# Kernel tuning notes

Measured on AMD Instinct MI355X. Metric: run time of the kernel, lower is better.

The kernel has to match this reference:

```python
import jax, jax.numpy as jnp
import numpy as np

DIM = 1024
NUM_HEADS = 16
NUM_KV_HEADS = 2
HEAD_DIM = DIM // NUM_HEADS          # 64
REPEATS = NUM_HEADS // NUM_KV_HEADS  # 8
WINDOW = 256
HALF = WINDOW // 2                   # 128
BATCH, SEQ = 2, 2048


def setup_inputs() -> dict:
    key = jax.random.key(0)
    ks = jax.random.split(key, 9)
    sc = 1.0 / np.sqrt(DIM)
    return {
        "x":  jax.random.normal(ks[0], (BATCH, SEQ, DIM), jnp.float32),
        "Wq": jax.random.normal(ks[1], (DIM, NUM_HEADS * HEAD_DIM), jnp.float32) * sc,
        "bq": jax.random.normal(ks[2], (NUM_HEADS * HEAD_DIM,), jnp.float32) * 0.01,
        "Wk": jax.random.normal(ks[3], (DIM, NUM_KV_HEADS * HEAD_DIM), jnp.float32) * sc,
        "bk": jax.random.normal(ks[4], (NUM_KV_HEADS * HEAD_DIM,), jnp.float32) * 0.01,
        "Wv": jax.random.normal(ks[5], (DIM, NUM_KV_HEADS * HEAD_DIM), jnp.float32) * sc,
        "bv": jax.random.normal(ks[6], (NUM_KV_HEADS * HEAD_DIM,), jnp.float32) * 0.01,
        "Wo": jax.random.normal(ks[7], (DIM, DIM), jnp.float32) * sc,
        "bo": jax.random.normal(ks[8], (DIM,), jnp.float32) * 0.01,
    }


def reference(x, Wq, bq, Wk, bk, Wv, bv, Wo, bo):
    # Training-path GQA sliding-window attention (faithful to the torch module):
    #  - K/V zero-padded by HALF on each side of the sequence; window of size
    #    WINDOW centered on each query position (unfold with step 1).
    #  - NOTE (faithful): the original code builds mask = tril(ones)[-1], which is
    #    an all-ones row, so masked_fill is a no-op -> NO causal mask inside the
    #    window; padded positions contribute score 0 (not -inf) to the softmax.
    #  - NOTE (faithful): the training path does NOT scale scores by 1/sqrt(d).
    b, s, _ = x.shape
    q = (x @ Wq + bq).reshape(b, s, NUM_HEADS, HEAD_DIM).transpose(0, 2, 1, 3)      # [b,H,s,d]
    k = (x @ Wk + bk).reshape(b, s, NUM_KV_HEADS, HEAD_DIM).transpose(0, 2, 1, 3)   # [b,G,s,d]
    v = (x @ Wv + bv).reshape(b, s, NUM_KV_HEADS, HEAD_DIM).transpose(0, 2, 1, 3)

    kp = jnp.pad(k, ((0, 0), (0, 0), (HALF, HALF), (0, 0)))  # [b,G,s+W,d]
    vp = jnp.pad(v, ((0, 0), (0, 0), (HALF, HALF), (0, 0)))

    # window gather indices: window i covers padded positions [i, i+W)
    idx = jnp.arange(s)[:, None] + jnp.arange(WINDOW)[None, :]  # [s,W]
    k_win = kp[:, :, idx]  # [b,G,s,W,d]  (gather at kv-head granularity, not H)
    v_win = vp[:, :, idx]

    # group query heads by kv head: head h -> kv group h // REPEATS
    qg = q.reshape(b, NUM_KV_HEADS, REPEATS, s, HEAD_DIM)        # [b,G,r,s,d]
    scores = jnp.einsum('bgrsd,bgswd->bgrsw', qg, k_win)         # no scaling (faithful)
    probs = jax.nn.softmax(scores, axis=-1)
    out = jnp.einsum('bgrsw,bgswd->bgrsd', probs, v_win)         # [b,G,r,s,d]

    out = out.reshape(b, NUM_HEADS, s, HEAD_DIM).transpose(0, 2, 1, 3).reshape(b, s, DIM)
    return out @ Wo + bo
```

## Files before the change

kernel.cpp:

```cpp
#include <hip/hip_runtime.h>
#include <hip/hip_fp16.h>

typedef _Float16 h16;
typedef __attribute__((ext_vector_type(4))) _Float16 h16x4;
typedef __attribute__((ext_vector_type(8))) _Float16 h16x8;
typedef __attribute__((ext_vector_type(4))) float f32x4;

#define DIM   1024
#define SEQ   2048
#define NKV   2
#define HD    64
#define HALFW 128
#define NQKV  1280
#define SPAD  2304
#define KPS   (SPAD*HD)
#define KSTG  288
#define VSTR  312
#define PSTR  296
#define LOG2E 1.4426950408889634f

__global__ void preprocess_kernel(const float* __restrict__ x,
                                  const float* __restrict__ bq,
                                  const float* __restrict__ bk,
                                  const float* __restrict__ bv,
                                  const float* __restrict__ Wq,
                                  const float* __restrict__ Wk,
                                  const float* __restrict__ Wv,
                                  const float* __restrict__ Wo,
                                  h16* __restrict__ xh, float* __restrict__ bqkv,
                                  h16* __restrict__ wqkvt, h16* __restrict__ wot,
                                  h16* __restrict__ kpad, h16* __restrict__ vtpad)
{
    __shared__ float tile[32][33];
    const int tid = threadIdx.x;
    const int blk = blockIdx.x;
    if (blk < 2048) {
        int i = blk * 256 + tid;
        size_t base = (size_t)i * 8;
        float4 a = *(const float4*)(x + base);
        float4 b = *(const float4*)(x + base + 4);
        h16x8 o = { (h16)a.x,(h16)a.y,(h16)a.z,(h16)a.w,
                    (h16)b.x,(h16)b.y,(h16)b.z,(h16)b.w };
        *(h16x8*)(xh + base) = o;
        if (i < NQKV) {
            float v = (i < DIM) ? bq[i] * LOG2E
                                : (i < DIM+128 ? bk[i-DIM] : bv[i-DIM-128]);
            bqkv[i] = v;
        }
        return;
    }
    if (blk >= 4352) {
        int idx = (blk - 4352) * 256 + tid;
        h16x8 z8 = {};
        h16* dstb = (idx < 16384) ? kpad : vtpad;
        int i2 = idx & 16383;
        int bg = i2 >> 12, j = i2 & 4095;
        if (j < 2048) {
            size_t off;
            if (idx < 16384) {
                off = (j < 1024) ? (size_t)j*8 : (size_t)2176*HD + (size_t)(j-1024)*8;
            } else {
                int d = j >> 5, r = j & 31;
                off = (size_t)d*SPAD + ((r & 16) ? 2176 : 0) + (size_t)(r & 15)*8;
            }
            *(h16x8*)(dstb + (size_t)bg*KPS + off) = z8;
        }
        return;
    }
    const int tx = tid & 31, ty = tid >> 5;
    if (blk < 2048 + 1280) {
        int bid = blk - 2048;
        int n0 = (bid % 40) * 32, k0 = (bid / 40) * 32;
        const float* src; int ldn, noff; float scl;
        if (n0 < DIM)          { src = Wq; ldn = DIM; noff = n0; scl = LOG2E; }
        else if (n0 < DIM+128) { src = Wk; ldn = 128; noff = n0 - DIM; scl = 1.f; }
        else                   { src = Wv; ldn = 128; noff = n0 - DIM - 128; scl = 1.f; }
#pragma unroll
        for (int i = 0; i < 4; ++i)
            tile[ty + 8*i][tx] = src[(size_t)(k0 + ty + 8*i)*ldn + noff + tx] * scl;
        __syncthreads();
#pragma unroll
        for (int i = 0; i < 4; ++i)
            wqkvt[(size_t)(n0 + ty + 8*i)*DIM + k0 + tx] = (h16)tile[tx][ty + 8*i];
    } else {
        int bid = blk - 3328;
        int n0 = (bid % 32) * 32, k0 = (bid / 32) * 32;
#pragma unroll
        for (int i = 0; i < 4; ++i)
            tile[ty + 8*i][tx] = Wo[(size_t)(k0 + ty + 8*i)*DIM + n0 + tx];
        __syncthreads();
#pragma unroll
        for (int i = 0; i < 4; ++i)
            wot[(size_t)(n0 + ty + 8*i)*DIM + k0 + tx] = (h16)tile[tx][ty + 8*i];
    }
}

__global__ void vtrans_kernel(const h16* __restrict__ v, h16* __restrict__ vt)
{
    __shared__ h16 tile[32][33];
    const int s0 = blockIdx.x * 32, d0 = blockIdx.y * 32, bg = blockIdx.z;
    const h16* src = v  + (size_t)bg * SEQ * HD;
    h16*       dst = vt + (size_t)bg * KPS;
    const int tx = threadIdx.x & 31, ty = threadIdx.x >> 5;
#pragma unroll
    for (int i = 0; i < 4; ++i)
        tile[ty + 8*i][tx] = src[(size_t)(s0 + ty + 8*i)*HD + d0 + tx];
    __syncthreads();
#pragma unroll
    for (int i = 0; i < 4; ++i)
        dst[(size_t)(d0 + ty + 8*i)*SPAD + HALFW + s0 + tx] = tile[tx][ty + 8*i];
}

template<int MODE>
__global__ __launch_bounds__(256, 3)
void gemm_kernel(const h16* __restrict__ A, const h16* __restrict__ Bt,
                 const float* __restrict__ bias,
                 h16* __restrict__ qo, h16* __restrict__ ko, h16* __restrict__ vo,
                 float* __restrict__ co, int K, int nx)
{
    __shared__ __align__(16) h16 As[2][128*64];
    __shared__ __align__(16) h16 Bs[2][64*64];
    const int nwg = gridDim.x, bid = blockIdx.x;
    const int wg = (bid & 7) * (nwg >> 3) + (bid >> 3);
    const int m0 = (wg / nx) * 128, n0 = (wg % nx) * 64;
    const int tid = threadIdx.x, lane = tid & 63, wid = tid >> 6;
    const int wr = wid >> 1, wc = wid & 1;
    f32x4 acc[4][2] = {};

    auto stage = [&](int buf, int kk) {
#pragma unroll
        for (int i = 0; i < 4; ++i) {
            int slot = i*256 + tid;
            int row = slot >> 3;
            int scol = ((slot & 7) ^ (row & 7)) * 8;
            __builtin_amdgcn_global_load_lds(
                (const __attribute__((address_space(1))) void*)(A + (size_t)(m0 + row)*K + kk + scol),
                (__attribute__((address_space(3))) void*)(&As[buf][slot*8]), 16, 0, 0);
        }
#pragma unroll
        for (int i = 0; i < 2; ++i) {
            int slot = i*256 + tid;
            int row = slot >> 3;
            int scol = ((slot & 7) ^ (row & 7)) * 8;
            __builtin_amdgcn_global_load_lds(
                (const __attribute__((address_space(1))) void*)(Bt + (size_t)(n0 + row)*K + kk + scol),
                (__attribute__((address_space(3))) void*)(&Bs[buf][slot*8]), 16, 0, 0);
        }
    };
    auto compute = [&](int buf) {
#pragma unroll
        for (int k2 = 0; k2 < 2; ++k2) {
            h16x8 a[4], b[2];
#pragma unroll
            for (int mi = 0; mi < 4; ++mi) {
                int row = wr*64 + mi*16 + (lane & 15);
                int cc = (k2*4 + (lane >> 4)) ^ (row & 7);
                a[mi] = *(const h16x8*)(&As[buf][row*64 + cc*8]);
            }
#pragma unroll
            for (int ni = 0; ni < 2; ++ni) {
                int row = wc*32 + ni*16 + (lane & 15);
                int cc = (k2*4 + (lane >> 4)) ^ (row & 7);
                b[ni] = *(const h16x8*)(&Bs[buf][row*64 + cc*8]);
            }
#pragma unroll
            for (int mi = 0; mi < 4; ++mi)
#pragma unroll
                for (int ni = 0; ni < 2; ++ni)
                    acc[mi][ni] = __builtin_amdgcn_mfma_f32_16x16x32_f16(a[mi], b[ni], acc[mi][ni], 0, 0, 0);
        }
    };

    const int ns = K >> 6;
    stage(0, 0);
    int cur = 0;
    for (int i = 0; i < ns; ++i) {
        if (i < ns-1) {
            stage(cur ^ 1, (i+1) << 6);
            asm volatile("s_waitcnt vmcnt(6)" ::: "memory");
        } else {
            asm volatile("s_waitcnt vmcnt(0)" ::: "memory");
        }
        __builtin_amdgcn_s_barrier();
        __builtin_amdgcn_sched_barrier(0);
        compute(cur);
        if (i < ns-1) {
            __builtin_amdgcn_s_barrier();
            __builtin_amdgcn_sched_barrier(0);
        }
        cur ^= 1;
    }

#pragma unroll
    for (int ni = 0; ni < 2; ++ni) {
        int n = n0 + wc*32 + ni*16 + (lane & 15);
        float bv = bias[n];
#pragma unroll
        for (int mi = 0; mi < 4; ++mi) {
            int mb = m0 + wr*64 + mi*16 + (lane >> 4)*4;
#pragma unroll
            for (int r = 0; r < 4; ++r) {
                int m = mb + r;
                float v = acc[mi][ni][r] + bv;
                if (MODE == 1) {
                    co[(size_t)m*DIM + n] = v;
                } else {
                    h16 hv = (h16)v;
                    if (n < DIM) {
                        qo[(size_t)m*DIM + n] = hv;
                    } else {
                        int nn = n - DIM;
                        int bi2 = m >> 11, s = m & 2047;
                        int g = (nn & 127) >> 6, d = nn & 63;
                        if (nn < 128)
                            ko[((size_t)(bi2*NKV + g)*SPAD + s + HALFW)*HD + d] = hv;
                        else
                            vo[(((size_t)(bi2*NKV + g))*SEQ + s)*HD + d] = hv;
                    }
                }
            }
        }
    }
}

__global__ __launch_bounds__(512)
void attn_kernel(const h16* __restrict__ qb, const h16* __restrict__ kpad,
                 const h16* __restrict__ vtpad, h16* __restrict__ ob)
{
    extern __shared__ char smem[];
    h16* Ks  = (h16*)smem;
    h16* Vts = (h16*)(smem + 36864);
    h16* Ps  = (h16*)(smem + 76800);
    const int tid = threadIdx.x, lane = tid & 63, wid = tid >> 6;
    const int qt = blockIdx.x, g = blockIdx.y, bi = blockIdx.z;
    const int s0 = qt * 32;
    const h16* Kbase = kpad  + (size_t)(bi*NKV + g)*KPS + (size_t)s0*HD;
    const h16* Vbase = vtpad + (size_t)(bi*NKV + g)*KPS + s0;

    for (int slot = tid; slot < KSTG*8; slot += 512) {
        int row = slot >> 3, cc = slot & 7;
        h16x8 val = *(const h16x8*)(Kbase + (size_t)row*HD + cc*8);
        *(h16x8*)(Ks + row*64 + ((cc ^ (row & 7)) * 8)) = val;
    }
    for (int slot = tid; slot < 64*38; slot += 512) {
        int row = slot / 38, cc = slot - row*38;
        h16x8 val = *(const h16x8*)(Vbase + (size_t)row*SPAD + cc*8);
        *(h16x8*)(Vts + row*VSTR + cc*8) = val;
    }
    h16* P = Ps + wid * 16 * PSTR;
    for (int i = lane; i < 256; i += 64)
        P[(i >> 4)*PSTR + 272 + (i & 15)] = (h16)0;
    __syncthreads();

    const int h = g*8 + wid;
    const int colbase = lane & 15;
    const int rowbase = (lane >> 4) * 4;
    const int kg = rowbase;

    for (int strip = 0; strip < 2; ++strip) {
        const int ss0 = s0 + strip*16;
        h16x8 aq[2];
#pragma unroll
        for (int c = 0; c < 2; ++c)
            aq[c] = *(const h16x8*)(qb + ((size_t)(bi*SEQ + ss0 + colbase))*DIM
                                    + h*HD + c*32 + (lane >> 4)*8);

        f32x4 sc[17];
        __builtin_amdgcn_s_setprio(1);
#pragma unroll
        for (int t = 0; t < 17; ++t) {
            f32x4 z = {0.f,0.f,0.f,0.f};
#pragma unroll
            for (int c = 0; c < 2; ++c) {
                int key = strip*16 + t*16 + colbase;
                h16x8 kf = *(const h16x8*)(Ks + key*64 + (((c*4 + (lane >> 4)) ^ (key & 7)) * 8));
                z = __builtin_amdgcn_mfma_f32_16x16x32_f16(kf, aq[c], z, 0, 0, 0);
            }
            sc[t] = z;
        }
        __builtin_amdgcn_s_setprio(0);

        float mx = -1e30f;
#pragma unroll
        for (int r = 0; r < 4; ++r) {
            float v0  = (kg + r >= colbase) ? sc[0][r]  : -1e30f;
            float v16 = (kg + r <  colbase) ? sc[16][r] : -1e30f;
            sc[0][r] = v0; sc[16][r] = v16;
            mx = fmaxf(mx, fmaxf(v0, v16));
        }
#pragma unroll
        for (int t = 1; t < 16; ++t)
#pragma unroll
            for (int r = 0; r < 4; ++r) mx = fmaxf(mx, sc[t][r]);
        mx = fmaxf(mx, __shfl_xor(mx, 16));
        mx = fmaxf(mx, __shfl_xor(mx, 32));
        float sum = 0.f;
#pragma unroll
        for (int t = 0; t < 17; ++t)
#pragma unroll
            for (int r = 0; r < 4; ++r) {
                float p = exp2f(sc[t][r] - mx);
                sc[t][r] = p;
                sum += p;
            }
        sum += __shfl_xor(sum, 16);
        sum += __shfl_xor(sum, 32);
        float inv = 1.0f / sum;

#pragma unroll
        for (int t = 0; t < 17; ++t) {
            h16x4 pk = { (h16)(sc[t][0]*inv), (h16)(sc[t][1]*inv),
                         (h16)(sc[t][2]*inv), (h16)(sc[t][3]*inv) };
            *(h16x4*)(P + colbase*PSTR + t*16 + kg) = pk;
        }

        f32x4 ao[4] = {};
        __builtin_amdgcn_s_setprio(1);
#pragma unroll
        for (int c = 0; c < 9; ++c) {
            h16x8 pa = *(const h16x8*)(P + colbase*PSTR + c*32 + (lane >> 4)*8);
            int vcol = strip*16 + c*32 + (lane >> 4)*8;
#pragma unroll
            for (int t2 = 0; t2 < 4; ++t2) {
                h16x8 vb = *(const h16x8*)(Vts + (t2*16 + colbase)*VSTR + vcol);
                ao[t2] = __builtin_amdgcn_mfma_f32_16x16x32_f16(pa, vb, ao[t2], 0, 0, 0);
            }
        }
        __builtin_amdgcn_s_setprio(0);
#pragma unroll
        for (int t2 = 0; t2 < 4; ++t2)
#pragma unroll
            for (int r = 0; r < 4; ++r)
                ob[((size_t)(bi*SEQ + ss0 + rowbase + r))*DIM + h*HD + t2*16 + colbase]
                    = (h16)ao[t2][r];
    }
}

extern "C" void kernel_launch(void* const* d_in, const int* in_sizes, int n_in,
                              void* d_out, int out_size, void* d_ws, size_t ws_size,
                              hipStream_t stream)
{
    const float* x  = (const float*)d_in[0];
    const float* Wq = (const float*)d_in[1];
    const float* bq = (const float*)d_in[2];
    const float* Wk = (const float*)d_in[3];
    const float* bk = (const float*)d_in[4];
    const float* Wv = (const float*)d_in[5];
    const float* bv = (const float*)d_in[6];
    const float* Wo = (const float*)d_in[7];
    const float* bo = (const float*)d_in[8];
    float* out = (float*)d_out;
    char* ws = (char*)d_ws;

    h16*   xh    = (h16*)(ws);
    h16*   wqkvt = (h16*)(ws + 8388608);
    h16*   wot   = (h16*)(ws + 11010048);
    float* bqkv  = (float*)(ws + 13107200);
    h16*   q_b   = (h16*)(ws + 13112320);
    h16*   k_pad = (h16*)(ws + 21500928);
    h16*   vt_pad= (h16*)(ws + 22680576);
    h16*   att_b = (h16*)(ws + 23860224);
    h16*   v_b   = att_b;

    preprocess_kernel<<<4480, 256, 0, stream>>>(x, bq, bk, bv, Wq, Wk, Wv, Wo,
                                                xh, bqkv, wqkvt, wot, k_pad, vt_pad);
    gemm_kernel<0><<<640, 256, 0, stream>>>(xh, wqkvt, bqkv,
                                            q_b, k_pad, v_b, nullptr, DIM, 20);
    vtrans_kernel<<<dim3(64, 2, 4), 256, 0, stream>>>(v_b, vt_pad);
    hipFuncSetAttribute((const void*)attn_kernel,
                        hipFuncAttributeMaxDynamicSharedMemorySize, 152576);
    attn_kernel<<<dim3(64, 2, 2), 512, 152576, stream>>>(q_b, k_pad, vt_pad, att_b);
    gemm_kernel<1><<<512, 256, 0, stream>>>(att_b, wot, bo,
                                            nullptr, nullptr, nullptr, out, DIM, 16);
}
```

Before: 67.37 us.

## Use 32x32x16 MFMA in attention and keep probabilities in registers

The attention kernel now covers all 32 queries of a block in one pass with 32x32x16 MFMA tiles instead of two 16-row strips with 16x16x32 tiles. Softmax probabilities are packed to fp16 in registers and exchanged across half-waves with shuffles to form the A operand, so the shared-memory P staging buffer is gone. The V tile gets an XOR swizzle instead of padding, which shrinks dynamic shared memory from about 149KB to 76KB and may let two blocks share a CU. In exchange the kernel holds many more live registers (9 f32x16 score tiles plus 72 packed words), which risks spills or lower occupancy.

After: 72.88 us. +8.2%, slower.

```diff
diff --git a/kernel.cpp b/kernel.cpp
--- a/kernel.cpp
+++ b/kernel.cpp
@@ -5,6 +5,8 @@
 typedef __attribute__((ext_vector_type(4))) _Float16 h16x4;
 typedef __attribute__((ext_vector_type(8))) _Float16 h16x8;
 typedef __attribute__((ext_vector_type(4))) float f32x4;
+typedef __attribute__((ext_vector_type(16))) float f32x16;
+typedef __attribute__((ext_vector_type(4))) unsigned u32x4;
 
 #define DIM   1024
 #define SEQ   2048
@@ -14,9 +16,6 @@
 #define NQKV  1280
 #define SPAD  2304
 #define KPS   (SPAD*HD)
-#define KSTG  288
-#define VSTR  312
-#define PSTR  296
 #define LOG2E 1.4426950408889634f
 
 __global__ void preprocess_kernel(const float* __restrict__ x,
@@ -230,109 +229,114 @@
     extern __shared__ char smem[];
     h16* Ks  = (h16*)smem;
     h16* Vts = (h16*)(smem + 36864);
-    h16* Ps  = (h16*)(smem + 76800);
     const int tid = threadIdx.x, lane = tid & 63, wid = tid >> 6;
     const int qt = blockIdx.x, g = blockIdx.y, bi = blockIdx.z;
     const int s0 = qt * 32;
     const h16* Kbase = kpad  + (size_t)(bi*NKV + g)*KPS + (size_t)s0*HD;
     const h16* Vbase = vtpad + (size_t)(bi*NKV + g)*KPS + s0;
 
-    for (int slot = tid; slot < KSTG*8; slot += 512) {
+    for (int slot = tid; slot < 288*8; slot += 512) {
         int row = slot >> 3, cc = slot & 7;
         h16x8 val = *(const h16x8*)(Kbase + (size_t)row*HD + cc*8);
         *(h16x8*)(Ks + row*64 + ((cc ^ (row & 7)) * 8)) = val;
     }
-    for (int slot = tid; slot < 64*38; slot += 512) {
-        int row = slot / 38, cc = slot - row*38;
+    for (int slot = tid; slot < 64*36; slot += 512) {
+        int row = slot / 36, cc = slot - row*36;
         h16x8 val = *(const h16x8*)(Vbase + (size_t)row*SPAD + cc*8);
-        *(h16x8*)(Vts + row*VSTR + cc*8) = val;
-    }
-    h16* P = Ps + wid * 16 * PSTR;
-    for (int i = lane; i < 256; i += 64)
-        P[(i >> 4)*PSTR + 272 + (i & 15)] = (h16)0;
+        *(h16x8*)(Vts + row*320 + ((cc ^ (row & 7)) * 8)) = val;
+    }
     __syncthreads();
 
     const int h = g*8 + wid;
-    const int colbase = lane & 15;
-    const int rowbase = (lane >> 4) * 4;
-    const int kg = rowbase;
-
-    for (int strip = 0; strip < 2; ++strip) {
-        const int ss0 = s0 + strip*16;
-        h16x8 aq[2];
-#pragma unroll
-        for (int c = 0; c < 2; ++c)
-            aq[c] = *(const h16x8*)(qb + ((size_t)(bi*SEQ + ss0 + colbase))*DIM
-                                    + h*HD + c*32 + (lane >> 4)*8);
-
-        f32x4 sc[17];
-        __builtin_amdgcn_s_setprio(1);
-#pragma unroll
-        for (int t = 0; t < 17; ++t) {
-            f32x4 z = {0.f,0.f,0.f,0.f};
-#pragma unroll
-            for (int c = 0; c < 2; ++c) {
-                int key = strip*16 + t*16 + colbase;
-                h16x8 kf = *(const h16x8*)(Ks + key*64 + (((c*4 + (lane >> 4)) ^ (key & 7)) * 8));
-                z = __builtin_amdgcn_mfma_f32_16x16x32_f16(kf, aq[c], z, 0, 0, 0);
-            }
-            sc[t] = z;
-        }
-        __builtin_amdgcn_s_setprio(0);
-
-        float mx = -1e30f;
-#pragma unroll
-        for (int r = 0; r < 4; ++r) {
-            float v0  = (kg + r >= colbase) ? sc[0][r]  : -1e30f;
-            float v16 = (kg + r <  colbase) ? sc[16][r] : -1e30f;
-            sc[0][r] = v0; sc[16][r] = v16;
-            mx = fmaxf(mx, fmaxf(v0, v16));
-        }
-#pragma unroll
-        for (int t = 1; t < 16; ++t)
-#pragma unroll
-            for (int r = 0; r < 4; ++r) mx = fmaxf(mx, sc[t][r]);
-        mx = fmaxf(mx, __shfl_xor(mx, 16));
-        mx = fmaxf(mx, __shfl_xor(mx, 32));
-        float sum = 0.f;
-#pragma unroll
-        for (int t = 0; t < 17; ++t)
-#pragma unroll
-            for (int r = 0; r < 4; ++r) {
-                float p = exp2f(sc[t][r] - mx);
-                sc[t][r] = p;
-                sum += p;
-            }
-        sum += __shfl_xor(sum, 16);
-        sum += __shfl_xor(sum, 32);
-        float inv = 1.0f / sum;
-
-#pragma unroll
-        for (int t = 0; t < 17; ++t) {
-            h16x4 pk = { (h16)(sc[t][0]*inv), (h16)(sc[t][1]*inv),
-                         (h16)(sc[t][2]*inv), (h16)(sc[t][3]*inv) };
-            *(h16x4*)(P + colbase*PSTR + t*16 + kg) = pk;
-        }
-
-        f32x4 ao[4] = {};
-        __builtin_amdgcn_s_setprio(1);
-#pragma unroll
-        for (int c = 0; c < 9; ++c) {
-            h16x8 pa = *(const h16x8*)(P + colbase*PSTR + c*32 + (lane >> 4)*8);
-            int vcol = strip*16 + c*32 + (lane >> 4)*8;
-#pragma unroll
-            for (int t2 = 0; t2 < 4; ++t2) {
-                h16x8 vb = *(const h16x8*)(Vts + (t2*16 + colbase)*VSTR + vcol);
-                ao[t2] = __builtin_amdgcn_mfma_f32_16x16x32_f16(pa, vb, ao[t2], 0, 0, 0);
-            }
-        }
-        __builtin_amdgcn_s_setprio(0);
-#pragma unroll
-        for (int t2 = 0; t2 < 4; ++t2)
-#pragma unroll
-            for (int r = 0; r < 4; ++r)
-                ob[((size_t)(bi*SEQ + ss0 + rowbase + r))*DIM + h*HD + t2*16 + colbase]
-                    = (h16)ao[t2][r];
+    const int q = lane & 31, hi2 = lane >> 5;
+
+    h16x8 aq[4];
+#pragma unroll
+    for (int c = 0; c < 4; ++c)
+        aq[c] = *(const h16x8*)(qb + ((size_t)(bi*SEQ + s0 + q))*DIM
+                                + h*HD + c*16 + hi2*8);
+
+    f32x16 sc[9];
+    __builtin_amdgcn_s_setprio(1);
+#pragma unroll
+    for (int T = 0; T < 9; ++T) {
+        f32x16 z = {};
+#pragma unroll
+        for (int c = 0; c < 4; ++c) {
+            int key = T*32 + q;
+            int chunk = (2*c + hi2) ^ (key & 7);
+            h16x8 kf = *(const h16x8*)(Ks + key*64 + chunk*8);
+            z = __builtin_amdgcn_mfma_f32_32x32x16_f16(kf, aq[c], z, 0, 0, 0);
+        }
+        sc[T] = z;
+    }
+    __builtin_amdgcn_s_setprio(0);
+
+    float mx = -1e30f;
+#pragma unroll
+    for (int r = 0; r < 16; ++r) {
+        int krow = (r & 3) + 8*(r >> 2) + 4*hi2;
+        float v0 = (krow >= q) ? sc[0][r] : -1e30f;
+        float v8 = (krow <  q) ? sc[8][r] : -1e30f;
+        sc[0][r] = v0; sc[8][r] = v8;
+        mx = fmaxf(mx, fmaxf(v0, v8));
+    }
+#pragma unroll
+    for (int T = 1; T < 8; ++T)
+#pragma unroll
+        for (int r = 0; r < 16; ++r) mx = fmaxf(mx, sc[T][r]);
+    mx = fmaxf(mx, __shfl_xor(mx, 32));
+    float sum = 0.f;
+#pragma unroll
+    for (int T = 0; T < 9; ++T)
+#pragma unroll
+        for (int r = 0; r < 16; ++r) {
+            float p = exp2f(sc[T][r] - mx);
+            sc[T][r] = p;
+            sum += p;
+        }
+    sum += __shfl_xor(sum, 32);
+    float inv = 1.0f / sum;
+
+    unsigned pk[72];
+#pragma unroll
+    for (int T = 0; T < 9; ++T)
+#pragma unroll
+        for (int p = 0; p < 8; ++p) {
+            h16 lo = (h16)(sc[T][2*p]   * inv);
+            h16 hi = (h16)(sc[T][2*p+1] * inv);
+            pk[T*8+p] = (unsigned)__builtin_bit_cast(unsigned short, lo)
+                      | ((unsigned)__builtin_bit_cast(unsigned short, hi) << 16);
+        }
+
+    f32x16 ao0 = {}, ao1 = {};
+    const bool hb = (hi2 != 0);
+    __builtin_amdgcn_s_setprio(1);
+#pragma unroll
+    for (int c = 0; c < 18; ++c) {
+        const int base = (c >> 1)*8 + (c & 1)*4;
+        unsigned D0 = pk[base], D1 = pk[base+1], D2 = pk[base+2], D3 = pk[base+3];
+        unsigned X0 = __shfl_xor(D0, 32), X1 = __shfl_xor(D1, 32);
+        unsigned X2 = __shfl_xor(D2, 32), X3 = __shfl_xor(D3, 32);
+        u32x4 pav = { hb ? X2 : D0, hb ? X3 : D1, hb ? D2 : X0, hb ? D3 : X1 };
+        h16x8 pa = __builtin_bit_cast(h16x8, pav);
+#pragma unroll
+        for (int dt = 0; dt < 2; ++dt) {
+            int d = dt*32 + q;
+            int chunk = (2*c + hi2) ^ (d & 7);
+            h16x8 vb = *(const h16x8*)(Vts + d*320 + chunk*8);
+            if (dt == 0) ao0 = __builtin_amdgcn_mfma_f32_32x32x16_f16(pa, vb, ao0, 0, 0, 0);
+            else         ao1 = __builtin_amdgcn_mfma_f32_32x32x16_f16(pa, vb, ao1, 0, 0, 0);
+        }
+    }
+    __builtin_amdgcn_s_setprio(0);
+
+#pragma unroll
+    for (int r = 0; r < 16; ++r) {
+        int qrow = (r & 3) + 8*(r >> 2) + 4*hi2;
+        size_t rowoff = ((size_t)(bi*SEQ + s0 + qrow))*DIM + h*HD;
+        ob[rowoff + q]      = (h16)ao0[r];
+        ob[rowoff + 32 + q] = (h16)ao1[r];
     }
 }
 
@@ -368,8 +372,8 @@
                                             q_b, k_pad, v_b, nullptr, DIM, 20);
     vtrans_kernel<<<dim3(64, 2, 4), 256, 0, stream>>>(v_b, vt_pad);
     hipFuncSetAttribute((const void*)attn_kernel,
-                        hipFuncAttributeMaxDynamicSharedMemorySize, 152576);
-    attn_kernel<<<dim3(64, 2, 2), 512, 152576, stream>>>(q_b, k_pad, vt_pad, att_b);
+                        hipFuncAttributeMaxDynamicSharedMemorySize, 77824);
+    attn_kernel<<<dim3(64, 2, 2), 512, 77824, stream>>>(q_b, k_pad, vt_pad, att_b);
     gemm_kernel<1><<<512, 256, 0, stream>>>(att_b, wot, bo,
                                             nullptr, nullptr, nullptr, out, DIM, 16);
 }
```
